# Kernel tuning notes

Measured on AMD Instinct MI355X. Metric: run time of the kernel, lower is better.

## Reference

```python
import jax, jax.numpy as jnp
import numpy as np

N = 50000   # nodes (cells)
E = 800000  # directed edges
D = 512     # input/output feature dim (genes)
H = D // 64 # bottleneck dim = 8
LN_EPS = 1e-5


def setup_inputs() -> dict:
    key = jax.random.key(0)
    ks = jax.random.split(key, 6)
    x = jax.random.normal(ks[0], (N, D), dtype=jnp.float32)
    edge_index = jax.random.randint(ks[1], (2, E), 0, N, dtype=jnp.int64)
    size_factors = jax.random.uniform(ks[2], (N, 1), dtype=jnp.float32) + 0.5
    s1 = float(1.0 / np.sqrt(D))
    W1 = jax.random.uniform(ks[3], (D, H), jnp.float32, -s1, s1)
    b1 = jnp.zeros((H,), jnp.float32)
    gamma = jnp.ones((H,), jnp.float32)
    beta = jnp.zeros((H,), jnp.float32)
    s2 = float(1.0 / np.sqrt(H))
    W2 = jax.random.uniform(ks[4], (H, D), jnp.float32, -s2, s2)
    b2 = jnp.zeros((D,), jnp.float32)
    return {"x": x, "size_factors": size_factors, "W1": W1, "b1": b1,
            "gamma": gamma, "beta": beta, "W2": W2, "b2": b2,
            "edge_index": edge_index}


def _gcn_conv(x, W, b, src, dst, norm):
    # PyG GCNConv: linear transform, then sym-normalized scatter-add aggregation.
    h = x @ W                                   # [N, out]
    msg = h[src] * norm[:, None]                # [E+N, out] gather + scale
    out = jax.ops.segment_sum(msg, dst, num_segments=N)  # scatter-add
    return out + b


def reference(x, size_factors, W1, b1, gamma, beta, W2, b2, edge_index):
    loops = jnp.arange(N, dtype=edge_index.dtype)
    src = jnp.concatenate([edge_index[0], loops])  # add self-loops
    dst = jnp.concatenate([edge_index[1], loops])
    deg = jax.ops.segment_sum(jnp.ones_like(src, dtype=x.dtype), dst,
                              num_segments=N)       # deg >= 1 via self-loops
    dinv = jax.lax.rsqrt(deg)
    norm = dinv[src] * dinv[dst]                    # [E+N]

    h = _gcn_conv(x, W1, b1, src, dst, norm)        # [N, H]
    mu = jnp.mean(h, axis=-1, keepdims=True)
    var = jnp.var(h, axis=-1, keepdims=True)
    h = (h - mu) * jax.lax.rsqrt(var + LN_EPS) * gamma + beta
    h = jax.nn.relu(h)
    # dropout p=0.0 -> identity
    out = jax.nn.relu(_gcn_conv(h, W2, b2, src, dst, norm))  # [N, D]
    return out * size_factors
```

## Files before the change

### kernel.cpp

```cpp
#include <hip/hip_runtime.h>

#define NN 50000
#define EE 800000
#define DD 512
#define HH 8
#define BA 160
#define CHUNK 5000
#define NBIN 196
#define BCAP 4608
#define GBLK 782
#define NTILE 3125
#define AGBLK 1563

typedef short bf16x8 __attribute__((ext_vector_type(8)));
typedef float f32x4 __attribute__((ext_vector_type(4)));

union U16 { uint4 u; bf16x8 v; unsigned short h[8]; };

__device__ __forceinline__ unsigned short f2bf(float f) {
    union { float f; unsigned int i; } c; c.f = f;
    unsigned int i = c.i;
    i += 0x7fffu + ((i >> 16) & 1u);
    return (unsigned short)(i >> 16);
}

__global__ __launch_bounds__(256) void k_gemm1_hist(const float4* __restrict__ x4,
                                                    const float* __restrict__ W1,
                                                    const int* __restrict__ dst,
                                                    float* __restrict__ t1,
                                                    int* __restrict__ blockhist) {
    __shared__ int smem[4096];
    int t = threadIdx.x;
    if (blockIdx.x >= GBLK) {
        int blk = blockIdx.x - GBLK;
        int* h = smem;
        h[t] = 0; __syncthreads();
        int base = blk * CHUNK;
#pragma unroll
        for (int it = 0; it < 20; ++it) {
            int i = it * 256 + t;
            if (i < CHUNK) atomicAdd(&h[dst[base + i] >> 8], 1);
        }
        __syncthreads();
        blockhist[blk * 256 + t] = h[t];
        return;
    }
    unsigned short* sbf = (unsigned short*)smem;
    for (int i = t; i < 16 * 64 * 8; i += 256) {
        int lane = (i >> 3) & 63, j = i & 7;
        int n = lane & 15;
        int k = (i >> 9) * 32 + ((lane >> 4) * 8) + j;
        sbf[i] = (n < HH) ? f2bf(W1[k * HH + n]) : (unsigned short)0;
    }
    __syncthreads();
    int wave = t >> 6, lane = t & 63;
    int tile = blockIdx.x * 4 + wave;
    if (tile >= NTILE) return;
    int node0 = tile * 16;
    int m = lane & 15, q = lane >> 4;
    const float4* xrow = x4 + (size_t)(node0 + m) * (DD / 4) + q * 2;
    const uint4* bfrag = (const uint4*)sbf;
    f32x4 acc = {0.f, 0.f, 0.f, 0.f};

    float4 bufA[8], bufB[8];
#define LOADG(buf, g)                                                      \
    _Pragma("unroll")                                                      \
    for (int s = 0; s < 4; ++s) {                                          \
        buf[2 * s]     = xrow[((g) * 4 + s) * 8];                          \
        buf[2 * s + 1] = xrow[((g) * 4 + s) * 8 + 1];                      \
    }
#define MFMAG(buf, g)                                                      \
    _Pragma("unroll")                                                      \
    for (int s = 0; s < 4; ++s) {                                          \
        U16 a, b;                                                          \
        float4 u0 = buf[2 * s], u1 = buf[2 * s + 1];                       \
        a.h[0] = f2bf(u0.x); a.h[1] = f2bf(u0.y);                          \
        a.h[2] = f2bf(u0.z); a.h[3] = f2bf(u0.w);                          \
        a.h[4] = f2bf(u1.x); a.h[5] = f2bf(u1.y);                          \
        a.h[6] = f2bf(u1.z); a.h[7] = f2bf(u1.w);                          \
        b.u = bfrag[((g) * 4 + s) * 64 + lane];                            \
        acc = __builtin_amdgcn_mfma_f32_16x16x32_bf16(a.v, b.v, acc, 0, 0, 0); \
    }
    LOADG(bufA, 0)
    LOADG(bufB, 1)
    MFMAG(bufA, 0)
    LOADG(bufA, 2)
    MFMAG(bufB, 1)
    LOADG(bufB, 3)
    MFMAG(bufA, 2)
    MFMAG(bufB, 3)
#undef LOADG
#undef MFMAG
    if (m < HH) {
        int base = (node0 + q * 4) * HH + m;
        t1[base]          = acc[0];
        t1[base + HH]     = acc[1];
        t1[base + 2 * HH] = acc[2];
        t1[base + 3 * HH] = acc[3];
    }
}

__global__ __launch_bounds__(256) void k_scan(int* __restrict__ blockhist,
                                              int* __restrict__ binBase,
                                              int* __restrict__ row) {
    __shared__ int s[256];
    int t = threadIdx.x;
    int sum = 0;
    for (int b = 0; b < BA; ++b) sum += blockhist[b * 256 + t];
    s[t] = sum; __syncthreads();
    for (int off = 1; off < 256; off <<= 1) {
        int x = (t >= off) ? s[t - off] : 0;
        __syncthreads();
        if (t >= off) s[t] += x;
        __syncthreads();
    }
    int excl = s[t] - sum;
    binBase[t] = excl;
    if (t == 255) { binBase[256] = s[255]; row[NN] = s[255]; }
    int run = excl;
    for (int b = 0; b < BA; ++b) {
        int v = blockhist[b * 256 + t];
        blockhist[b * 256 + t] = run;
        run += v;
    }
}

__global__ __launch_bounds__(256) void k_scatter(const int* __restrict__ eidx,
                                                 const int* __restrict__ blockhist,
                                                 int* __restrict__ bucket) {
    __shared__ int cur[256];
    int t = threadIdx.x, blk = blockIdx.x;
    cur[t] = blockhist[blk * 256 + t]; __syncthreads();
    int base = blk * CHUNK;
#pragma unroll
    for (int it = 0; it < 20; ++it) {
        int i = it * 256 + t;
        if (i < CHUNK) {
            int s = eidx[base + i], d = eidx[EE + base + i];
            int pos = atomicAdd(&cur[d >> 8], 1);
            bucket[pos] = (s << 8) | (d & 255);
        }
    }
}

__global__ __launch_bounds__(256) void k_build(const int* __restrict__ bucket,
                                               const int* __restrict__ binBase,
                                               int* __restrict__ row,
                                               int* __restrict__ adj,
                                               float* __restrict__ dinvA) {
    __shared__ int smem[2 * BCAP + 768];
    int t = threadIdx.x;
    int bin = blockIdx.x;
    int n0 = bin << 8;
    int segStart = binBase[bin];
    int count = binBase[bin + 1] - segStart;
    if (count > BCAP) count = BCAP;
    int* lds_in  = smem;
    int* lds_out = smem + BCAP;
    int* cnt     = smem + 2 * BCAP;
    int* off     = smem + 2 * BCAP + 256;
    int* cur2    = smem + 2 * BCAP + 512;
    cnt[t] = 0; __syncthreads();
    for (int i = t; i < count; i += 256) {
        int p = bucket[segStart + i];
        lds_in[i] = p;
        atomicAdd(&cnt[p & 255], 1);
    }
    __syncthreads();
    off[t] = cnt[t]; __syncthreads();
    for (int o = 1; o < 256; o <<= 1) {
        int x = (t >= o) ? off[t - o] : 0;
        __syncthreads();
        if (t >= o) off[t] += x;
        __syncthreads();
    }
    int excl = off[t] - cnt[t];
    cur2[t] = excl;
    int n = n0 + t;
    if (n < NN) {
        row[n] = segStart + excl;
        dinvA[n] = rsqrtf((float)cnt[t] + 1.0f);
    }
    __syncthreads();
    for (int i = t; i < count; i += 256) {
        int p = lds_in[i];
        int pos = atomicAdd(&cur2[p & 255], 1);
        lds_out[pos] = p >> 8;
    }
    __syncthreads();
    for (int i = t; i < count; i += 256)
        adj[segStart + i] = lds_out[i];
}

__global__ __launch_bounds__(256) void k_agg1(const float* __restrict__ t1,
                                              const int* __restrict__ row,
                                              const int* __restrict__ adj,
                                              const float* __restrict__ dinvA,
                                              const float* __restrict__ b1,
                                              const float* __restrict__ gma,
                                              const float* __restrict__ bta,
                                              float* __restrict__ h2) {
    int gid = blockIdx.x * 256 + threadIdx.x;
    int n = gid >> 3, f = gid & 7;
    if (n >= NN) return;
    int beg = row[n], end = row[n + 1];
    float dv = dinvA[n];
    float acc = t1[(size_t)n * HH + f] * dv;
    int i = beg;
    for (; i + 2 <= end; i += 2) {
        int s0 = adj[i], s1 = adj[i + 1];
        float w0 = dinvA[s0], w1 = dinvA[s1];
        acc += t1[(size_t)s0 * HH + f] * w0;
        acc += t1[(size_t)s1 * HH + f] * w1;
    }
    if (i < end) {
        int s0 = adj[i];
        acc += t1[(size_t)s0 * HH + f] * dinvA[s0];
    }
    acc = acc * dv + b1[f];
    float s = acc;
    s += __shfl_xor(s, 1); s += __shfl_xor(s, 2); s += __shfl_xor(s, 4);
    float mu = s * 0.125f;
    float dx = acc - mu;
    float sq = dx * dx;
    sq += __shfl_xor(sq, 1); sq += __shfl_xor(sq, 2); sq += __shfl_xor(sq, 4);
    float rs = rsqrtf(sq * 0.125f + 1e-5f);
    h2[(size_t)n * HH + f] = fmaxf(dx * rs * gma[f] + bta[f], 0.f);
}

__global__ __launch_bounds__(256) void k_agg2_gemm2(const float* __restrict__ h2,
                                                    const int* __restrict__ row,
                                                    const int* __restrict__ adj,
                                                    const float* __restrict__ dinvA,
                                                    const float* __restrict__ W2,
                                                    const float* __restrict__ b2,
                                                    const float* __restrict__ sf,
                                                    float* __restrict__ out) {
    __shared__ float sA[32 * 8];
    int tid = threadIdx.x;
    int c = tid & 63, g = tid >> 6, d0 = c * 8;
    float w[8][8];
#pragma unroll
    for (int k = 0; k < 8; ++k) {
        float4 u0 = *(const float4*)(W2 + k * DD + d0);
        float4 u1 = *(const float4*)(W2 + k * DD + d0 + 4);
        w[k][0] = u0.x; w[k][1] = u0.y; w[k][2] = u0.z; w[k][3] = u0.w;
        w[k][4] = u1.x; w[k][5] = u1.y; w[k][6] = u1.z; w[k][7] = u1.w;
    }
    float bb[8];
    {
        float4 u0 = *(const float4*)(b2 + d0);
        float4 u1 = *(const float4*)(b2 + d0 + 4);
        bb[0] = u0.x; bb[1] = u0.y; bb[2] = u0.z; bb[3] = u0.w;
        bb[4] = u1.x; bb[5] = u1.y; bb[6] = u1.z; bb[7] = u1.w;
    }
    int nl = tid >> 3, f = tid & 7;
    int n = blockIdx.x * 32 + nl;
    if (n < NN) {
        int beg = row[n], end = row[n + 1];
        float dv = dinvA[n];
        float acc = h2[(size_t)n * HH + f] * dv;
        int i = beg;
        for (; i + 2 <= end; i += 2) {
            int s0 = adj[i], s1 = adj[i + 1];
            float w0 = dinvA[s0], w1 = dinvA[s1];
            acc += h2[(size_t)s0 * HH + f] * w0;
            acc += h2[(size_t)s1 * HH + f] * w1;
        }
        if (i < end) {
            int s0 = adj[i];
            acc += h2[(size_t)s0 * HH + f] * dinvA[s0];
        }
        sA[nl * 8 + f] = acc * dv;
    }
    __syncthreads();
#pragma unroll
    for (int i = 0; i < 8; ++i) {
        int rrow = i * 4 + g;
        int n2 = blockIdx.x * 32 + rrow;
        if (n2 < NN) {
            float a[8];
#pragma unroll
            for (int j = 0; j < 8; ++j) a[j] = sA[rrow * 8 + j];
            float s = sf[n2];
            float acc[8];
#pragma unroll
            for (int j = 0; j < 8; ++j) acc[j] = bb[j];
#pragma unroll
            for (int k = 0; k < 8; ++k)
#pragma unroll
                for (int j = 0; j < 8; ++j) acc[j] += a[k] * w[k][j];
            float4 o0 = make_float4(fmaxf(acc[0], 0.f) * s, fmaxf(acc[1], 0.f) * s,
                                    fmaxf(acc[2], 0.f) * s, fmaxf(acc[3], 0.f) * s);
            float4 o1 = make_float4(fmaxf(acc[4], 0.f) * s, fmaxf(acc[5], 0.f) * s,
                                    fmaxf(acc[6], 0.f) * s, fmaxf(acc[7], 0.f) * s);
            float4* op = (float4*)(out + (size_t)n2 * DD + d0);
            op[0] = o0;
            op[1] = o1;
        }
    }
}

extern "C" void kernel_launch(void* const* d_in, const int* in_sizes, int n_in,
                              void* d_out, int out_size, void* d_ws, size_t ws_size,
                              hipStream_t stream) {
    (void)in_sizes; (void)n_in; (void)out_size; (void)ws_size;
    const float* x   = (const float*)d_in[0];
    const float* sf  = (const float*)d_in[1];
    const float* W1  = (const float*)d_in[2];
    const float* b1  = (const float*)d_in[3];
    const float* gma = (const float*)d_in[4];
    const float* bta = (const float*)d_in[5];
    const float* W2  = (const float*)d_in[6];
    const float* b2  = (const float*)d_in[7];
    const int* eidx  = (const int*)d_in[8];
    float* out = (float*)d_out;

    char* ws = (char*)d_ws;
    int*   blockhist = (int*)(ws + 0);
    int*   binBase   = (int*)(ws + 262144);
    int*   row       = (int*)(ws + (1 << 20));
    float* dinvA     = (float*)(ws + 2 * (1 << 20));
    float* t1        = (float*)(ws + 3 * (1 << 20));
    float* h2        = (float*)(ws + 5 * (1 << 20));
    int*   adj       = (int*)(ws + 7 * (1 << 20));
    int*   bucket    = (int*)(ws + 11 * (1 << 20));

    k_gemm1_hist<<<GBLK + BA, 256, 0, stream>>>((const float4*)x, W1, eidx + EE,
                                                t1, blockhist);
    k_scan<<<1, 256, 0, stream>>>(blockhist, binBase, row);
    k_scatter<<<BA, 256, 0, stream>>>(eidx, blockhist, bucket);
    k_build<<<NBIN, 256, 0, stream>>>(bucket, binBase, row, adj, dinvA);
    k_agg1<<<AGBLK, 256, 0, stream>>>(t1, row, adj, dinvA, b1, gma, bta, h2);
    k_agg2_gemm2<<<AGBLK, 256, 0, stream>>>(h2, row, adj, dinvA, W2, b2, sf, out);
}
```

Before: 280.4 us.

## Parallelize histogram scan across bins and unroll aggregation gather loops by four

Replaces the single-block scan, which looped serially over 160 block histograms per bin, with a per-bin parallel scan kernel (256 blocks) and then a small scan over bin totals. The scatter kernel now adds the bin base to the per-block offset. The neighbor gather loops in both aggregation kernels are unrolled by four so more independent loads are in flight. This adds one extra kernel launch and a few more registers in exchange for shorter serial latency in the scan and better memory-level parallelism in the gathers.

```diff
diff --git a/kernel.cpp b/kernel.cpp
--- a/kernel.cpp
+++ b/kernel.cpp
@@ -11,6 +11,7 @@
 #define GBLK 782
 #define NTILE 3125
 #define AGBLK 1563
+#define SCANT 192
 
 typedef short bf16x8 __attribute__((ext_vector_type(8)));
 typedef float f32x4 __attribute__((ext_vector_type(4)));
@@ -100,37 +101,46 @@
     }
 }
 
-__global__ __launch_bounds__(256) void k_scan(int* __restrict__ blockhist,
-                                              int* __restrict__ binBase,
-                                              int* __restrict__ row) {
+__global__ __launch_bounds__(SCANT) void k_scan_a(int* __restrict__ blockhist,
+                                                  int* __restrict__ binTotal) {
+    __shared__ int s[SCANT];
+    int bin = blockIdx.x, t = threadIdx.x;
+    int v = (t < BA) ? blockhist[t * 256 + bin] : 0;
+    s[t] = v; __syncthreads();
+    for (int off = 1; off < SCANT; off <<= 1) {
+        int x = (t >= off) ? s[t - off] : 0;
+        __syncthreads();
+        if (t >= off) s[t] += x;
+        __syncthreads();
+    }
+    if (t < BA) blockhist[t * 256 + bin] = s[t] - v;
+    if (t == SCANT - 1) binTotal[bin] = s[t];
+}
+
+__global__ __launch_bounds__(256) void k_scan_b(const int* __restrict__ binTotal,
+                                                int* __restrict__ binBase,
+                                                int* __restrict__ row) {
     __shared__ int s[256];
     int t = threadIdx.x;
-    int sum = 0;
-    for (int b = 0; b < BA; ++b) sum += blockhist[b * 256 + t];
-    s[t] = sum; __syncthreads();
+    int v = binTotal[t];
+    s[t] = v; __syncthreads();
     for (int off = 1; off < 256; off <<= 1) {
         int x = (t >= off) ? s[t - off] : 0;
         __syncthreads();
         if (t >= off) s[t] += x;
         __syncthreads();
     }
-    int excl = s[t] - sum;
-    binBase[t] = excl;
+    binBase[t] = s[t] - v;
     if (t == 255) { binBase[256] = s[255]; row[NN] = s[255]; }
-    int run = excl;
-    for (int b = 0; b < BA; ++b) {
-        int v = blockhist[b * 256 + t];
-        blockhist[b * 256 + t] = run;
-        run += v;
-    }
 }
 
 __global__ __launch_bounds__(256) void k_scatter(const int* __restrict__ eidx,
                                                  const int* __restrict__ blockhist,
+                                                 const int* __restrict__ binBase,
                                                  int* __restrict__ bucket) {
     __shared__ int cur[256];
     int t = threadIdx.x, blk = blockIdx.x;
-    cur[t] = blockhist[blk * 256 + t]; __syncthreads();
+    cur[t] = binBase[t] + blockhist[blk * 256 + t]; __syncthreads();
     int base = blk * CHUNK;
 #pragma unroll
     for (int it = 0; it < 20; ++it) {
@@ -207,13 +217,14 @@
     float dv = dinvA[n];
     float acc = t1[(size_t)n * HH + f] * dv;
     int i = beg;
-    for (; i + 2 <= end; i += 2) {
-        int s0 = adj[i], s1 = adj[i + 1];
-        float w0 = dinvA[s0], w1 = dinvA[s1];
-        acc += t1[(size_t)s0 * HH + f] * w0;
-        acc += t1[(size_t)s1 * HH + f] * w1;
-    }
-    if (i < end) {
+    for (; i + 4 <= end; i += 4) {
+        int s0 = adj[i], s1 = adj[i + 1], s2 = adj[i + 2], s3 = adj[i + 3];
+        float w0 = dinvA[s0], w1 = dinvA[s1], w2 = dinvA[s2], w3 = dinvA[s3];
+        float v0 = t1[(size_t)s0 * HH + f], v1 = t1[(size_t)s1 * HH + f];
+        float v2 = t1[(size_t)s2 * HH + f], v3 = t1[(size_t)s3 * HH + f];
+        acc += v0 * w0 + v1 * w1 + v2 * w2 + v3 * w3;
+    }
+    for (; i < end; ++i) {
         int s0 = adj[i];
         acc += t1[(size_t)s0 * HH + f] * dinvA[s0];
     }
@@ -261,13 +272,14 @@
         float dv = dinvA[n];
         float acc = h2[(size_t)n * HH + f] * dv;
         int i = beg;
-        for (; i + 2 <= end; i += 2) {
-            int s0 = adj[i], s1 = adj[i + 1];
-            float w0 = dinvA[s0], w1 = dinvA[s1];
-            acc += h2[(size_t)s0 * HH + f] * w0;
-            acc += h2[(size_t)s1 * HH + f] * w1;
-        }
-        if (i < end) {
+        for (; i + 4 <= end; i += 4) {
+            int s0 = adj[i], s1 = adj[i + 1], s2 = adj[i + 2], s3 = adj[i + 3];
+            float w0 = dinvA[s0], w1 = dinvA[s1], w2 = dinvA[s2], w3 = dinvA[s3];
+            float v0 = h2[(size_t)s0 * HH + f], v1 = h2[(size_t)s1 * HH + f];
+            float v2 = h2[(size_t)s2 * HH + f], v3 = h2[(size_t)s3 * HH + f];
+            acc += v0 * w0 + v1 * w1 + v2 * w2 + v3 * w3;
+        }
+        for (; i < end; ++i) {
             int s0 = adj[i];
             acc += h2[(size_t)s0 * HH + f] * dinvA[s0];
         }
@@ -319,6 +331,7 @@
     char* ws = (char*)d_ws;
     int*   blockhist = (int*)(ws + 0);
     int*   binBase   = (int*)(ws + 262144);
+    int*   binTotal  = (int*)(ws + 262144 + 2048);
     int*   row       = (int*)(ws + (1 << 20));
     float* dinvA     = (float*)(ws + 2 * (1 << 20));
     float* t1        = (float*)(ws + 3 * (1 << 20));
@@ -328,8 +341,9 @@
 
     k_gemm1_hist<<<GBLK + BA, 256, 0, stream>>>((const float4*)x, W1, eidx + EE,
                                                 t1, blockhist);
-    k_scan<<<1, 256, 0, stream>>>(blockhist, binBase, row);
-    k_scatter<<<BA, 256, 0, stream>>>(eidx, blockhist, bucket);
+    k_scan_a<<<256, SCANT, 0, stream>>>(blockhist, binTotal);
+    k_scan_b<<<1, 256, 0, stream>>>(binTotal, binBase, row);
+    k_scatter<<<BA, 256, 0, stream>>>(eidx, blockhist, binBase, bucket);
     k_build<<<NBIN, 256, 0, stream>>>(bucket, binBase, row, adj, dinvA);
     k_agg1<<<AGBLK, 256, 0, stream>>>(t1, row, adj, dinvA, b1, gma, bta, h2);
     k_agg2_gemm2<<<AGBLK, 256, 0, stream>>>(h2, row, adj, dinvA, W2, b2, sf, out);
```

New measurement: 273.7 us. 2.4% less time.

## Replace CSR build with fixed-capacity dst bins and LDS atomic aggregation

Applied to the files above, without the earlier changes.

Drops the histogram, scan and per-bin sort that built a CSR adjacency. Edges are now scattered into fixed-capacity buckets of 64 destination nodes using global atomics, and each aggregation block accumulates its bucket's messages with shared-memory float atomics. The source-side dinv scaling is folded into t1 and h2 ahead of time, so the gathers no longer do a per-edge dinv lookup. The cost is global atomic contention in the scatter, nondeterministic summation order, and dropped edges if any bin exceeds CAP=1280 (expected load is about 1024).

```diff
diff --git a/kernel.cpp b/kernel.cpp
--- a/kernel.cpp
+++ b/kernel.cpp
@@ -4,13 +4,10 @@
 #define EE 800000
 #define DD 512
 #define HH 8
-#define BA 160
-#define CHUNK 5000
-#define NBIN 196
-#define BCAP 4608
+#define NB 782
+#define CAP 1280
 #define GBLK 782
 #define NTILE 3125
-#define AGBLK 1563
 
 typedef short bf16x8 __attribute__((ext_vector_type(8)));
 typedef float f32x4 __attribute__((ext_vector_type(4)));
@@ -24,27 +21,11 @@
     return (unsigned short)(i >> 16);
 }
 
-__global__ __launch_bounds__(256) void k_gemm1_hist(const float4* __restrict__ x4,
-                                                    const float* __restrict__ W1,
-                                                    const int* __restrict__ dst,
-                                                    float* __restrict__ t1,
-                                                    int* __restrict__ blockhist) {
+__global__ __launch_bounds__(256) void k_gemm1(const float4* __restrict__ x4,
+                                               const float* __restrict__ W1,
+                                               float* __restrict__ t1) {
     __shared__ int smem[4096];
     int t = threadIdx.x;
-    if (blockIdx.x >= GBLK) {
-        int blk = blockIdx.x - GBLK;
-        int* h = smem;
-        h[t] = 0; __syncthreads();
-        int base = blk * CHUNK;
-#pragma unroll
-        for (int it = 0; it < 20; ++it) {
-            int i = it * 256 + t;
-            if (i < CHUNK) atomicAdd(&h[dst[base + i] >> 8], 1);
-        }
-        __syncthreads();
-        blockhist[blk * 256 + t] = h[t];
-        return;
-    }
     unsigned short* sbf = (unsigned short*)smem;
     for (int i = t; i < 16 * 64 * 8; i += 256) {
         int lane = (i >> 3) & 63, j = i & 7;
@@ -100,145 +81,117 @@
     }
 }
 
-__global__ __launch_bounds__(256) void k_scan(int* __restrict__ blockhist,
-                                              int* __restrict__ binBase,
-                                              int* __restrict__ row) {
-    __shared__ int s[256];
-    int t = threadIdx.x;
-    int sum = 0;
-    for (int b = 0; b < BA; ++b) sum += blockhist[b * 256 + t];
-    s[t] = sum; __syncthreads();
-    for (int off = 1; off < 256; off <<= 1) {
-        int x = (t >= off) ? s[t - off] : 0;
-        __syncthreads();
-        if (t >= off) s[t] += x;
-        __syncthreads();
-    }
-    int excl = s[t] - sum;
-    binBase[t] = excl;
-    if (t == 255) { binBase[256] = s[255]; row[NN] = s[255]; }
-    int run = excl;
-    for (int b = 0; b < BA; ++b) {
-        int v = blockhist[b * 256 + t];
-        blockhist[b * 256 + t] = run;
-        run += v;
-    }
-}
-
 __global__ __launch_bounds__(256) void k_scatter(const int* __restrict__ eidx,
-                                                 const int* __restrict__ blockhist,
+                                                 int* __restrict__ binCur,
                                                  int* __restrict__ bucket) {
-    __shared__ int cur[256];
-    int t = threadIdx.x, blk = blockIdx.x;
-    cur[t] = blockhist[blk * 256 + t]; __syncthreads();
-    int base = blk * CHUNK;
-#pragma unroll
-    for (int it = 0; it < 20; ++it) {
-        int i = it * 256 + t;
-        if (i < CHUNK) {
-            int s = eidx[base + i], d = eidx[EE + base + i];
-            int pos = atomicAdd(&cur[d >> 8], 1);
-            bucket[pos] = (s << 8) | (d & 255);
-        }
-    }
-}
-
-__global__ __launch_bounds__(256) void k_build(const int* __restrict__ bucket,
-                                               const int* __restrict__ binBase,
-                                               int* __restrict__ row,
-                                               int* __restrict__ adj,
-                                               float* __restrict__ dinvA) {
-    __shared__ int smem[2 * BCAP + 768];
-    int t = threadIdx.x;
-    int bin = blockIdx.x;
-    int n0 = bin << 8;
-    int segStart = binBase[bin];
-    int count = binBase[bin + 1] - segStart;
-    if (count > BCAP) count = BCAP;
-    int* lds_in  = smem;
-    int* lds_out = smem + BCAP;
-    int* cnt     = smem + 2 * BCAP;
-    int* off     = smem + 2 * BCAP + 256;
-    int* cur2    = smem + 2 * BCAP + 512;
-    cnt[t] = 0; __syncthreads();
-    for (int i = t; i < count; i += 256) {
-        int p = bucket[segStart + i];
-        lds_in[i] = p;
-        atomicAdd(&cnt[p & 255], 1);
-    }
-    __syncthreads();
-    off[t] = cnt[t]; __syncthreads();
-    for (int o = 1; o < 256; o <<= 1) {
-        int x = (t >= o) ? off[t - o] : 0;
-        __syncthreads();
-        if (t >= o) off[t] += x;
-        __syncthreads();
-    }
-    int excl = off[t] - cnt[t];
-    cur2[t] = excl;
-    int n = n0 + t;
-    if (n < NN) {
-        row[n] = segStart + excl;
-        dinvA[n] = rsqrtf((float)cnt[t] + 1.0f);
-    }
-    __syncthreads();
-    for (int i = t; i < count; i += 256) {
-        int p = lds_in[i];
-        int pos = atomicAdd(&cur2[p & 255], 1);
-        lds_out[pos] = p >> 8;
-    }
-    __syncthreads();
-    for (int i = t; i < count; i += 256)
-        adj[segStart + i] = lds_out[i];
+    int t = threadIdx.x, b = blockIdx.x;
+    int base = b * 1024;
+#pragma unroll
+    for (int it = 0; it < 4; ++it) {
+        int i = base + it * 256 + t;
+        if (i < EE) {
+            int s = eidx[i], d = eidx[EE + i];
+            int bin = d >> 6;
+            int pos = atomicAdd(&binCur[bin], 1);
+            if (pos < CAP) bucket[bin * CAP + pos] = (s << 6) | (d & 63);
+        }
+    }
+}
+
+__global__ __launch_bounds__(256) void k_dinv(const int* __restrict__ bucket,
+                                              const int* __restrict__ binCur,
+                                              float* __restrict__ dinvA,
+                                              float* __restrict__ t1) {
+    __shared__ int cnt[64];
+    __shared__ int cshare;
+    int t = threadIdx.x, b = blockIdx.x;
+    if (t < 64) cnt[t] = 0;
+    if (t == 0) { int c = binCur[b]; cshare = (c > CAP) ? CAP : c; }
+    __syncthreads();
+    int count = cshare;
+    const int* bk = bucket + b * CAP;
+    for (int i = t; i < count; i += 256) atomicAdd(&cnt[bk[i] & 63], 1);
+    __syncthreads();
+    if (t < 64) {
+        int n = (b << 6) + t;
+        if (n < NN) {
+            float dv = rsqrtf((float)cnt[t] + 1.0f);
+            dinvA[n] = dv;
+            float4* tp = (float4*)(t1 + (size_t)n * HH);
+            float4 a = tp[0], c = tp[1];
+            a.x *= dv; a.y *= dv; a.z *= dv; a.w *= dv;
+            c.x *= dv; c.y *= dv; c.z *= dv; c.w *= dv;
+            tp[0] = a; tp[1] = c;
+        }
+    }
 }
 
 __global__ __launch_bounds__(256) void k_agg1(const float* __restrict__ t1,
-                                              const int* __restrict__ row,
-                                              const int* __restrict__ adj,
+                                              const int* __restrict__ bucket,
+                                              const int* __restrict__ binCur,
                                               const float* __restrict__ dinvA,
                                               const float* __restrict__ b1,
                                               const float* __restrict__ gma,
                                               const float* __restrict__ bta,
                                               float* __restrict__ h2) {
-    int gid = blockIdx.x * 256 + threadIdx.x;
-    int n = gid >> 3, f = gid & 7;
-    if (n >= NN) return;
-    int beg = row[n], end = row[n + 1];
-    float dv = dinvA[n];
-    float acc = t1[(size_t)n * HH + f] * dv;
-    int i = beg;
-    for (; i + 2 <= end; i += 2) {
-        int s0 = adj[i], s1 = adj[i + 1];
-        float w0 = dinvA[s0], w1 = dinvA[s1];
-        acc += t1[(size_t)s0 * HH + f] * w0;
-        acc += t1[(size_t)s1 * HH + f] * w1;
-    }
-    if (i < end) {
-        int s0 = adj[i];
-        acc += t1[(size_t)s0 * HH + f] * dinvA[s0];
-    }
-    acc = acc * dv + b1[f];
-    float s = acc;
-    s += __shfl_xor(s, 1); s += __shfl_xor(s, 2); s += __shfl_xor(s, 4);
-    float mu = s * 0.125f;
-    float dx = acc - mu;
-    float sq = dx * dx;
-    sq += __shfl_xor(sq, 1); sq += __shfl_xor(sq, 2); sq += __shfl_xor(sq, 4);
-    float rs = rsqrtf(sq * 0.125f + 1e-5f);
-    h2[(size_t)n * HH + f] = fmaxf(dx * rs * gma[f] + bta[f], 0.f);
-}
-
-__global__ __launch_bounds__(256) void k_agg2_gemm2(const float* __restrict__ h2,
-                                                    const int* __restrict__ row,
-                                                    const int* __restrict__ adj,
-                                                    const float* __restrict__ dinvA,
-                                                    const float* __restrict__ W2,
-                                                    const float* __restrict__ b2,
-                                                    const float* __restrict__ sf,
-                                                    float* __restrict__ out) {
-    __shared__ float sA[32 * 8];
-    int tid = threadIdx.x;
-    int c = tid & 63, g = tid >> 6, d0 = c * 8;
+    __shared__ float acc[64 * 9];
+    __shared__ int cshare;
+    int t = threadIdx.x, b = blockIdx.x;
+    int n0 = b << 6;
+    for (int i = t; i < 512; i += 256) {
+        int nl = i >> 3, f = i & 7;
+        int n = n0 + nl;
+        acc[nl * 9 + f] = (n < NN) ? t1[(size_t)n * HH + f] : 0.f;
+    }
+    if (t == 0) { int c = binCur[b]; cshare = (c > CAP) ? CAP : c; }
+    __syncthreads();
+    int count = cshare;
+    const int* bk = bucket + b * CAP;
+    for (int i = t; i < count; i += 256) {
+        int p = bk[i];
+        int s = p >> 6, dl = p & 63;
+        const float4* sp = (const float4*)(t1 + (size_t)s * HH);
+        float4 u0 = sp[0], u1 = sp[1];
+        float* a = &acc[dl * 9];
+        atomicAdd(a + 0, u0.x); atomicAdd(a + 1, u0.y);
+        atomicAdd(a + 2, u0.z); atomicAdd(a + 3, u0.w);
+        atomicAdd(a + 4, u1.x); atomicAdd(a + 5, u1.y);
+        atomicAdd(a + 6, u1.z); atomicAdd(a + 7, u1.w);
+    }
+    __syncthreads();
+    int nl2 = t >> 3, f = t & 7;
+#pragma unroll
+    for (int pass = 0; pass < 2; ++pass) {
+        int nl = pass * 32 + nl2;
+        int n = n0 + nl;
+        if (n < NN) {
+            float dv = dinvA[n];
+            float v = acc[nl * 9 + f] * dv + b1[f];
+            float s = v;
+            s += __shfl_xor(s, 1); s += __shfl_xor(s, 2); s += __shfl_xor(s, 4);
+            float mu = s * 0.125f;
+            float dx = v - mu;
+            float sq = dx * dx;
+            sq += __shfl_xor(sq, 1); sq += __shfl_xor(sq, 2); sq += __shfl_xor(sq, 4);
+            float rs = rsqrtf(sq * 0.125f + 1e-5f);
+            h2[(size_t)n * HH + f] = fmaxf(dx * rs * gma[f] + bta[f], 0.f) * dv;
+        }
+    }
+}
+
+__global__ __launch_bounds__(256) void k_agg2(const float* __restrict__ h2,
+                                              const int* __restrict__ bucket,
+                                              const int* __restrict__ binCur,
+                                              const float* __restrict__ dinvA,
+                                              const float* __restrict__ W2,
+                                              const float* __restrict__ b2,
+                                              const float* __restrict__ sf,
+                                              float* __restrict__ out) {
+    __shared__ float acc[64 * 9];
+    __shared__ int cshare;
+    int t = threadIdx.x, b = blockIdx.x;
+    int n0 = b << 6;
+    int c = t & 63, g = t >> 6, d0 = c * 8;
     float w[8][8];
 #pragma unroll
     for (int k = 0; k < 8; ++k) {
@@ -254,46 +207,53 @@
         bb[0] = u0.x; bb[1] = u0.y; bb[2] = u0.z; bb[3] = u0.w;
         bb[4] = u1.x; bb[5] = u1.y; bb[6] = u1.z; bb[7] = u1.w;
     }
-    int nl = tid >> 3, f = tid & 7;
-    int n = blockIdx.x * 32 + nl;
-    if (n < NN) {
-        int beg = row[n], end = row[n + 1];
-        float dv = dinvA[n];
-        float acc = h2[(size_t)n * HH + f] * dv;
-        int i = beg;
-        for (; i + 2 <= end; i += 2) {
-            int s0 = adj[i], s1 = adj[i + 1];
-            float w0 = dinvA[s0], w1 = dinvA[s1];
-            acc += h2[(size_t)s0 * HH + f] * w0;
-            acc += h2[(size_t)s1 * HH + f] * w1;
-        }
-        if (i < end) {
-            int s0 = adj[i];
-            acc += h2[(size_t)s0 * HH + f] * dinvA[s0];
-        }
-        sA[nl * 8 + f] = acc * dv;
-    }
-    __syncthreads();
-#pragma unroll
-    for (int i = 0; i < 8; ++i) {
-        int rrow = i * 4 + g;
-        int n2 = blockIdx.x * 32 + rrow;
+    for (int i = t; i < 512; i += 256) {
+        int nl = i >> 3, f = i & 7;
+        int n = n0 + nl;
+        acc[nl * 9 + f] = (n < NN) ? h2[(size_t)n * HH + f] : 0.f;
+    }
+    if (t == 0) { int cc = binCur[b]; cshare = (cc > CAP) ? CAP : cc; }
+    __syncthreads();
+    int count = cshare;
+    const int* bk = bucket + b * CAP;
+    for (int i = t; i < count; i += 256) {
+        int p = bk[i];
+        int s = p >> 6, dl = p & 63;
+        const float4* sp = (const float4*)(h2 + (size_t)s * HH);
+        float4 u0 = sp[0], u1 = sp[1];
+        float* a = &acc[dl * 9];
+        atomicAdd(a + 0, u0.x); atomicAdd(a + 1, u0.y);
+        atomicAdd(a + 2, u0.z); atomicAdd(a + 3, u0.w);
+        atomicAdd(a + 4, u1.x); atomicAdd(a + 5, u1.y);
+        atomicAdd(a + 6, u1.z); atomicAdd(a + 7, u1.w);
+    }
+    __syncthreads();
+    for (int i = t; i < 512; i += 256) {
+        int nl = i >> 3, f = i & 7;
+        int n = n0 + nl;
+        if (n < NN) acc[nl * 9 + f] *= dinvA[n];
+    }
+    __syncthreads();
+#pragma unroll
+    for (int it = 0; it < 16; ++it) {
+        int rrow = it * 4 + g;
+        int n2 = n0 + rrow;
         if (n2 < NN) {
             float a[8];
 #pragma unroll
-            for (int j = 0; j < 8; ++j) a[j] = sA[rrow * 8 + j];
+            for (int j = 0; j < 8; ++j) a[j] = acc[rrow * 9 + j];
             float s = sf[n2];
-            float acc[8];
-#pragma unroll
-            for (int j = 0; j < 8; ++j) acc[j] = bb[j];
+            float o[8];
+#pragma unroll
+            for (int j = 0; j < 8; ++j) o[j] = bb[j];
 #pragma unroll
             for (int k = 0; k < 8; ++k)
 #pragma unroll
-                for (int j = 0; j < 8; ++j) acc[j] += a[k] * w[k][j];
-            float4 o0 = make_float4(fmaxf(acc[0], 0.f) * s, fmaxf(acc[1], 0.f) * s,
-                                    fmaxf(acc[2], 0.f) * s, fmaxf(acc[3], 0.f) * s);
-            float4 o1 = make_float4(fmaxf(acc[4], 0.f) * s, fmaxf(acc[5], 0.f) * s,
-                                    fmaxf(acc[6], 0.f) * s, fmaxf(acc[7], 0.f) * s);
+                for (int j = 0; j < 8; ++j) o[j] += a[k] * w[k][j];
+            float4 o0 = make_float4(fmaxf(o[0], 0.f) * s, fmaxf(o[1], 0.f) * s,
+                                    fmaxf(o[2], 0.f) * s, fmaxf(o[3], 0.f) * s);
+            float4 o1 = make_float4(fmaxf(o[4], 0.f) * s, fmaxf(o[5], 0.f) * s,
+                                    fmaxf(o[6], 0.f) * s, fmaxf(o[7], 0.f) * s);
             float4* op = (float4*)(out + (size_t)n2 * DD + d0);
             op[0] = o0;
             op[1] = o1;
@@ -317,20 +277,16 @@
     float* out = (float*)d_out;
 
     char* ws = (char*)d_ws;
-    int*   blockhist = (int*)(ws + 0);
-    int*   binBase   = (int*)(ws + 262144);
-    int*   row       = (int*)(ws + (1 << 20));
-    float* dinvA     = (float*)(ws + 2 * (1 << 20));
-    float* t1        = (float*)(ws + 3 * (1 << 20));
-    float* h2        = (float*)(ws + 5 * (1 << 20));
-    int*   adj       = (int*)(ws + 7 * (1 << 20));
-    int*   bucket    = (int*)(ws + 11 * (1 << 20));
-
-    k_gemm1_hist<<<GBLK + BA, 256, 0, stream>>>((const float4*)x, W1, eidx + EE,
-                                                t1, blockhist);
-    k_scan<<<1, 256, 0, stream>>>(blockhist, binBase, row);
-    k_scatter<<<BA, 256, 0, stream>>>(eidx, blockhist, bucket);
-    k_build<<<NBIN, 256, 0, stream>>>(bucket, binBase, row, adj, dinvA);
-    k_agg1<<<AGBLK, 256, 0, stream>>>(t1, row, adj, dinvA, b1, gma, bta, h2);
-    k_agg2_gemm2<<<AGBLK, 256, 0, stream>>>(h2, row, adj, dinvA, W2, b2, sf, out);
-}
+    int*   binCur = (int*)(ws + 0);
+    float* dinvA  = (float*)(ws + (1 << 20));
+    float* t1     = (float*)(ws + 2 * (1 << 20));
+    float* h2     = (float*)(ws + 4 * (1 << 20));
+    int*   bucket = (int*)(ws + 6 * (1 << 20));
+
+    hipMemsetAsync(binCur, 0, NB * sizeof(int), stream);
+    k_gemm1<<<GBLK, 256, 0, stream>>>((const float4*)x, W1, t1);
+    k_scatter<<<NB, 256, 0, stream>>>(eidx, binCur, bucket);
+    k_dinv<<<NB, 256, 0, stream>>>(bucket, binCur, dinvA, t1);
+    k_agg1<<<NB, 256, 0, stream>>>(t1, bucket, binCur, dinvA, b1, gma, bta, h2);
+    k_agg2<<<NB, 256, 0, stream>>>(h2, bucket, binCur, dinvA, W2, b2, sf, out);
+}
```

Measured after the change: 508.9 us. +81.5%, slower.
